# Optimization experiments

Hardware: AMD Instinct MI355X
Metric: run time of the kernel (lower is better)

The kernel has to match this reference:

```python
import jax, jax.numpy as jnp
import numpy as np

NP, NA = 60000, 30000          # paper / author node counts
EC, EW, EB = 300000, 150000, 150000
IN_F, HID, H, D, NCLS = 1024, 512, 4, 128, 153  # HID = H*D


def setup_inputs() -> dict:
    key = jax.random.key(0)
    ks = jax.random.split(key, 24)
    inp = {
        "x_paper": jax.random.normal(ks[0], (NP, IN_F), jnp.float32),
        "x_author": jax.random.normal(ks[1], (NA, IN_F), jnp.float32),
        "cites_src": jax.random.randint(ks[2], (EC,), 0, NP, jnp.int32),
        "cites_dst": jax.random.randint(ks[3], (EC,), 0, NP, jnp.int32),
        "writes_src": jax.random.randint(ks[4], (EW,), 0, NA, jnp.int32),
        "writes_dst": jax.random.randint(ks[5], (EW,), 0, NP, jnp.int32),
        "wb_src": jax.random.randint(ks[6], (EB,), 0, NP, jnp.int32),
        "wb_dst": jax.random.randint(ks[7], (EB,), 0, NA, jnp.int32),
        "W0": jax.random.normal(ks[8], (3, IN_F, HID), jnp.float32) * 0.02,
        "al0": jax.random.normal(ks[9], (3, H, D), jnp.float32) * 0.1,
        "ar0": jax.random.normal(ks[10], (3, H, D), jnp.float32) * 0.1,
        "W1": jax.random.normal(ks[11], (3, HID, HID), jnp.float32) * 0.03,
        "al1": jax.random.normal(ks[12], (3, H, D), jnp.float32) * 0.1,
        "ar1": jax.random.normal(ks[13], (3, H, D), jnp.float32) * 0.1,
        "W2": jax.random.normal(ks[14], (3, HID, HID), jnp.float32) * 0.03,
        "al2": jax.random.normal(ks[15], (3, H, D), jnp.float32) * 0.1,
        "ar2": jax.random.normal(ks[16], (3, H, D), jnp.float32) * 0.1,
        "linW": jax.random.normal(ks[17], (HID, NCLS), jnp.float32) * 0.02,
        "linb": jnp.zeros((NCLS,), jnp.float32),
    }
    return inp


def gat_conv(h_src, h_dst, src, dst, W, al, ar, n_dst):
    """DGL-style GATConv on one edge type (bipartite block, shared fc)."""
    zs = (h_src @ W).reshape(-1, H, D)            # (Ns,H,D)
    zd = (h_dst @ W).reshape(-1, H, D)            # (Nd,H,D)
    el = jnp.sum(zs * al, axis=-1)                # (Ns,H)
    er = jnp.sum(zd * ar, axis=-1)                # (Nd,H)
    e = jax.nn.leaky_relu(el[src] + er[dst], 0.2)  # (E,H)
    # edge softmax over incoming edges per destination node
    m = jax.ops.segment_max(e, dst, num_segments=n_dst)
    m = jnp.where(jnp.isfinite(m), m, 0.0)
    ee = jnp.exp(e - m[dst])
    s = jax.ops.segment_sum(ee, dst, num_segments=n_dst)
    a = ee / (s[dst] + 1e-9)                      # (E,H)
    # weighted message aggregation: (Nd,H,D)
    return jax.ops.segment_sum(a[:, :, None] * zs[src], dst, num_segments=n_dst)


def reference(x_paper, x_author, cites_src, cites_dst, writes_src, writes_dst,
              wb_src, wb_dst, W0, al0, ar0, W1, al1, ar1, W2, al2, ar2,
              linW, linb):
    def hetero_layer(hp, ha, W, al, ar, act):
        # HeteroGraphConv: sum-aggregate per destination node type
        op = (gat_conv(hp, hp, cites_src, cites_dst, W[0], al[0], ar[0], NP)
              + gat_conv(ha, hp, writes_src, writes_dst, W[1], al[1], ar[1], NP))
        oa = gat_conv(hp, ha, wb_src, wb_dst, W[2], al[2], ar[2], NA)
        op = op.reshape(NP, H * D)   # head-flatten as in forward()
        oa = oa.reshape(NA, H * D)
        if act:
            op, oa = jax.nn.relu(op), jax.nn.relu(oa)
        return op, oa

    hp, ha = x_paper, x_author
    hp, ha = hetero_layer(hp, ha, W0, al0, ar0, True)
    hp, ha = hetero_layer(hp, ha, W1, al1, ar1, True)
    hp, ha = hetero_layer(hp, ha, W2, al2, ar2, False)  # last layer: no activation
    return hp @ linW + linb
```

## Files before the change

kernel.cpp:

```cpp
#include <hip/hip_runtime.h>
#include <cstddef>
#include <cstdint>

static constexpr int NP = 60000, NA = 30000;
static constexpr int EC = 300000, EW = 150000, EB = 150000;
static constexpr int IN_F = 1024, HID = 512, H = 4, D = 128, NCLS = 153;
static constexpr int MPAD_P = 60160;
static constexpr int MPAD_A = 30208;

typedef __attribute__((ext_vector_type(8))) short short8;
typedef __attribute__((ext_vector_type(4))) float float4v;

__device__ __forceinline__ unsigned short f2bf(float f) {
    unsigned int u = __float_as_uint(f);
    unsigned int r = u + 0x7FFFu + ((u >> 16) & 1u);
    return (unsigned short)(r >> 16);
}
__device__ __forceinline__ float bf2f(unsigned short h) {
    return __uint_as_float(((unsigned int)h) << 16);
}

__device__ __forceinline__ void gll16(const unsigned short* g, unsigned short* l) {
    __builtin_amdgcn_global_load_lds(
        (const __attribute__((address_space(1))) unsigned int*)g,
        (__attribute__((address_space(3))) unsigned int*)l, 16, 0, 0);
}

__global__ void hist_kernel(const int* __restrict__ dst, int E, int* __restrict__ counts) {
    int e = blockIdx.x * 256 + threadIdx.x;
    if (e < E) atomicAdd(&counts[dst[e]], 1);
}

__global__ void exscan_kernel(const int* __restrict__ in, int* __restrict__ out, int n) {
    __shared__ int wsum[4];
    int t = threadIdx.x;
    int lane = t & 63, w = t >> 6;
    int carry = 0;
    const int CH = 256 * 8;
    for (int base = 0; base < n; base += CH) {
        int v[8], run[8];
        int i0 = base + t * 8;
        int tsum = 0;
#pragma unroll
        for (int j = 0; j < 8; ++j) {
            int i = i0 + j;
            v[j] = (i < n) ? in[i] : 0;
            tsum += v[j];
            run[j] = tsum;
        }
        int x = tsum;
#pragma unroll
        for (int off = 1; off < 64; off <<= 1) {
            int y = __shfl_up(x, off);
            if (lane >= off) x += y;
        }
        if (lane == 63) wsum[w] = x;
        __syncthreads();
        int wpre = 0;
        for (int ww = 0; ww < w; ++ww) wpre += wsum[ww];
        int chunktot = wsum[0] + wsum[1] + wsum[2] + wsum[3];
        int pre = carry + wpre + (x - tsum);
#pragma unroll
        for (int j = 0; j < 8; ++j) {
            int i = i0 + j;
            if (i < n) out[i] = pre + run[j] - v[j];
        }
        carry += chunktot;
        __syncthreads();
    }
    if (t == 0) out[n] = carry;
}

__global__ void fill_kernel(const int* __restrict__ src, const int* __restrict__ dst, int E,
                            int* __restrict__ cursor, int* __restrict__ col) {
    int e = blockIdx.x * 256 + threadIdx.x;
    if (e < E) {
        int pos = atomicAdd(&cursor[dst[e]], 1);
        col[pos] = src[e];
    }
}

__global__ void decomp4_kernel(const float4* __restrict__ x, ushort4* __restrict__ hi,
                               ushort4* __restrict__ lo, int M, int K, int Mpad) {
    size_t i4 = (size_t)blockIdx.x * 256 + threadIdx.x;
    size_t tot = ((size_t)Mpad * K) >> 2;
    if (i4 >= tot) return;
    size_t row = (i4 * 4) / (size_t)K;
    float4 v = make_float4(0.f, 0.f, 0.f, 0.f);
    if (row < (size_t)M) v = x[i4];
    ushort4 h, l;
    h.x = f2bf(v.x); h.y = f2bf(v.y); h.z = f2bf(v.z); h.w = f2bf(v.w);
    l.x = f2bf(v.x - bf2f(h.x)); l.y = f2bf(v.y - bf2f(h.y));
    l.z = f2bf(v.z - bf2f(h.z)); l.w = f2bf(v.w - bf2f(h.w));
    hi[i4] = h; lo[i4] = l;
}

__global__ void btprep_kernel(const float* __restrict__ W, unsigned short* __restrict__ hi,
                              unsigned short* __restrict__ lo, int K, int N, int Npad) {
    int i = blockIdx.x * 256 + threadIdx.x;
    if (i >= Npad * K) return;
    int n = i / K, k = i - n * K;
    float v = (n < N) ? W[(size_t)k * N + n] : 0.f;
    unsigned short h = f2bf(v);
    hi[i] = h;
    lo[i] = f2bf(v - bf2f(h));
}

__global__ __launch_bounds__(512, 2) void gemm_ring(
    const unsigned short* __restrict__ Ahi, const unsigned short* __restrict__ Alo,
    const unsigned short* __restrict__ Bhi, const unsigned short* __restrict__ Blo,
    const float* __restrict__ bias, float* __restrict__ C,
    int M, int K, int Nstore, int ldc) {
    extern __shared__ unsigned short lds[];
    const int tid = threadIdx.x;
    const int lane = tid & 63;
    const int w = tid >> 6;
    const int wr = w >> 2, wc = w & 3;
    const int bm = blockIdx.y * 256, bn = blockIdx.x * 256;

    const int st_row = w * 16 + (lane >> 2);
    const int st_sc = (((lane & 3) ^ ((lane >> 3) & 3)) << 3);
    const size_t aoff0 = (size_t)(bm + st_row) * K + st_sc;
    const size_t aoff1 = aoff0 + (size_t)128 * K;
    const size_t boff0 = (size_t)(bn + st_row) * K + st_sc;
    const size_t boff1 = boff0 + (size_t)128 * K;
    const int ldsA = w * 512;
    const int ldsB = 8192 + w * 512;

    const int arow = wr * 128 + (lane & 15);
    const int brow = wc * 64 + (lane & 15);
    const int rq = ((((lane >> 4) & 3) ^ ((lane >> 1) & 3)) << 3);
    const int aRead = arow * 32 + rq;
    const int bRead = 8192 + brow * 32 + rq;

    float4v acc[8][4];
    float4v zf = {0.f, 0.f, 0.f, 0.f};
#pragma unroll
    for (int i = 0; i < 8; ++i)
#pragma unroll
        for (int j = 0; j < 4; ++j) acc[i][j] = zf;

    auto STAGE = [&](unsigned rr, const unsigned short* As, const unsigned short* Bs, int kc) {
        unsigned short* sb = &lds[rr * 16384u];
        gll16(As + aoff0 + kc, sb + ldsA);
        gll16(As + aoff1 + kc, sb + ldsA + 4096);
        gll16(Bs + boff0 + kc, sb + ldsB);
        gll16(Bs + boff1 + kc, sb + ldsB + 4096);
    };
    auto COMPUTE = [&](unsigned rr) {
        const unsigned short* sb = &lds[rr * 16384u];
        short8 fa[8], fb[4];
#pragma unroll
        for (int i = 0; i < 8; ++i) fa[i] = *(const short8*)&sb[aRead + i * 512];
#pragma unroll
        for (int j = 0; j < 4; ++j) fb[j] = *(const short8*)&sb[bRead + j * 512];
        __builtin_amdgcn_s_setprio(1);
#pragma unroll
        for (int i = 0; i < 8; ++i)
#pragma unroll
            for (int j = 0; j < 4; ++j)
                acc[i][j] = __builtin_amdgcn_mfma_f32_16x16x32_bf16(fa[i], fb[j], acc[i][j], 0, 0, 0);
        __builtin_amdgcn_s_setprio(0);
    };

#define WAITV(n) asm volatile("s_waitcnt vmcnt(" #n ")" ::: "memory")
#define BARF()                                 \
    do {                                       \
        asm volatile("" ::: "memory");         \
        __builtin_amdgcn_s_barrier();          \
        asm volatile("" ::: "memory");         \
    } while (0)

    STAGE(0, Ahi, Bhi, 0);
    STAGE(1, Alo, Bhi, 0);
    STAGE(2, Ahi, Blo, 0);
    unsigned rg = 0;
    const int nK = K >> 5;
#pragma unroll 1
    for (int t3 = 0; t3 < nK - 1; ++t3) {
        const int kn = (t3 + 1) << 5;
        STAGE((rg + 3) & 3, Ahi, Bhi, kn);
        WAITV(12);
        BARF();
        COMPUTE(rg);
        BARF();
        rg = (rg + 1) & 3;
        STAGE((rg + 3) & 3, Alo, Bhi, kn);
        WAITV(12);
        BARF();
        COMPUTE(rg);
        BARF();
        rg = (rg + 1) & 3;
        STAGE((rg + 3) & 3, Ahi, Blo, kn);
        WAITV(12);
        BARF();
        COMPUTE(rg);
        BARF();
        rg = (rg + 1) & 3;
    }
    WAITV(8);
    BARF();
    COMPUTE(rg);
    BARF();
    rg = (rg + 1) & 3;
    WAITV(4);
    BARF();
    COMPUTE(rg);
    BARF();
    rg = (rg + 1) & 3;
    WAITV(0);
    BARF();
    COMPUTE(rg);
#undef WAITV
#undef BARF

    const int col0 = bn + wc * 64 + (lane & 15);
    const int row0 = bm + wr * 128 + ((lane >> 4) << 2);
#pragma unroll
    for (int i = 0; i < 8; ++i) {
#pragma unroll
        for (int j = 0; j < 4; ++j) {
            int col = col0 + j * 16;
            if (col >= Nstore) continue;
            float badd = bias ? bias[col] : 0.f;
            int rowb = row0 + i * 16;
#pragma unroll
            for (int k = 0; k < 4; ++k) {
                int row = rowb + k;
                if (row < M) C[(size_t)row * ldc + col] = acc[i][j][k] + badd;
            }
        }
    }
}

__global__ __launch_bounds__(256) void eler_kernel(
    const float* __restrict__ z, const float* __restrict__ al, const float* __restrict__ ar,
    float* __restrict__ el, float* __restrict__ er, int M) {
    int row = blockIdx.x * 4 + (threadIdx.x >> 6);
    int lane = threadIdx.x & 63;
    if (row >= M) return;
    const float4* zr = (const float4*)(z + (size_t)row * 512 + lane * 8);
    float4 z0 = zr[0], z1 = zr[1];
    const float4* alp = (const float4*)(al + lane * 8);
    float4 a0 = alp[0], a1 = alp[1];
    float s = z0.x * a0.x + z0.y * a0.y + z0.z * a0.z + z0.w * a0.w
            + z1.x * a1.x + z1.y * a1.y + z1.z * a1.z + z1.w * a1.w;
    s += __shfl_xor(s, 8); s += __shfl_xor(s, 4); s += __shfl_xor(s, 2); s += __shfl_xor(s, 1);
    int h = lane >> 4;
    if ((lane & 15) == 0) el[(size_t)row * 4 + h] = s;
    if (er) {
        const float4* arp = (const float4*)(ar + lane * 8);
        float4 b0 = arp[0], b1 = arp[1];
        float t = z0.x * b0.x + z0.y * b0.y + z0.z * b0.z + z0.w * b0.w
                + z1.x * b1.x + z1.y * b1.y + z1.z * b1.z + z1.w * b1.w;
        t += __shfl_xor(t, 8); t += __shfl_xor(t, 4); t += __shfl_xor(t, 2); t += __shfl_xor(t, 1);
        if ((lane & 15) == 0) er[(size_t)row * 4 + h] = t;
    }
}

__global__ void fold_kernel(const float* __restrict__ W, const float* __restrict__ ar,
                            float* __restrict__ v, int K) {
    int i = blockIdx.x * 256 + threadIdx.x;
    if (i >= K * 4) return;
    int k = i >> 2, h = i & 3;
    const float* wr = W + (size_t)k * 512 + h * 128;
    const float* a = ar + h * 128;
    float s = 0.f;
#pragma unroll 4
    for (int d = 0; d < 128; ++d) s += wr[d] * a[d];
    v[i] = s;
}

__global__ __launch_bounds__(256) void skinny_kernel(
    const float* __restrict__ h, const float* __restrict__ v,
    float* __restrict__ er, int M, int K) {
    __shared__ float vs[4096];
    for (int i = threadIdx.x; i < K * 4; i += 256) vs[i] = v[i];
    __syncthreads();
    int row = blockIdx.x * 4 + (threadIdx.x >> 6);
    int lane = threadIdx.x & 63;
    if (row >= M) return;
    const float* hr = h + (size_t)row * K;
    float a0 = 0, a1 = 0, a2 = 0, a3 = 0;
    for (int k = lane; k < K; k += 64) {
        float x = hr[k];
        float4 vv = *(const float4*)&vs[k * 4];
        a0 += x * vv.x; a1 += x * vv.y; a2 += x * vv.z; a3 += x * vv.w;
    }
#pragma unroll
    for (int off = 32; off; off >>= 1) {
        a0 += __shfl_xor(a0, off); a1 += __shfl_xor(a1, off);
        a2 += __shfl_xor(a2, off); a3 += __shfl_xor(a3, off);
    }
    if (lane == 0) *(float4*)&er[(size_t)row * 4] = make_float4(a0, a1, a2, a3);
}

__global__ __launch_bounds__(256) void agg_fused(
    const int* __restrict__ rp1, const int* __restrict__ col1, const float* __restrict__ z1,
    const float* __restrict__ el1, const float* __restrict__ er1,
    const int* __restrict__ rp2, const int* __restrict__ col2, const float* __restrict__ z2,
    const float* __restrict__ el2, const float* __restrict__ er2,
    float* __restrict__ out, unsigned short* __restrict__ hi, unsigned short* __restrict__ lo,
    int N, int do_relu) {
    int j = blockIdx.x * 4 + (threadIdx.x >> 6);
    int lane = threadIdx.x & 63;
    if (j >= N) return;
    int h = lane >> 4;
    float4 acc0 = make_float4(0, 0, 0, 0), acc1 = make_float4(0, 0, 0, 0);

    {
        int e0 = rp1[j], e1 = rp1[j + 1];
        float erh = er1[(size_t)j * 4 + h];
        float m = -INFINITY, s = 0.f;
        for (int e = e0; e < e1; ++e) {
            float x = el1[(size_t)col1[e] * 4 + h] + erh;
            x = (x >= 0.f) ? x : 0.2f * x;
            float mn = fmaxf(m, x);
            s = s * expf(m - mn) + expf(x - mn);
            m = mn;
        }
        float inv = 1.0f / (s + 1e-9f);
        for (int e = e0; e < e1; ++e) {
            int src = col1[e];
            float x = el1[(size_t)src * 4 + h] + erh;
            x = (x >= 0.f) ? x : 0.2f * x;
            float wgt = expf(x - m) * inv;
            const float4* zr = (const float4*)(z1 + (size_t)src * 512 + lane * 8);
            float4 za = zr[0], zb = zr[1];
            acc0.x += wgt * za.x; acc0.y += wgt * za.y; acc0.z += wgt * za.z; acc0.w += wgt * za.w;
            acc1.x += wgt * zb.x; acc1.y += wgt * zb.y; acc1.z += wgt * zb.z; acc1.w += wgt * zb.w;
        }
    }
    if (rp2) {
        int e0 = rp2[j], e1 = rp2[j + 1];
        float erh = er2[(size_t)j * 4 + h];
        float m = -INFINITY, s = 0.f;
        for (int e = e0; e < e1; ++e) {
            float x = el2[(size_t)col2[e] * 4 + h] + erh;
            x = (x >= 0.f) ? x : 0.2f * x;
            float mn = fmaxf(m, x);
            s = s * expf(m - mn) + expf(x - mn);
            m = mn;
        }
        float inv = 1.0f / (s + 1e-9f);
        for (int e = e0; e < e1; ++e) {
            int src = col2[e];
            float x = el2[(size_t)src * 4 + h] + erh;
            x = (x >= 0.f) ? x : 0.2f * x;
            float wgt = expf(x - m) * inv;
            const float4* zr = (const float4*)(z2 + (size_t)src * 512 + lane * 8);
            float4 za = zr[0], zb = zr[1];
            acc0.x += wgt * za.x; acc0.y += wgt * za.y; acc0.z += wgt * za.z; acc0.w += wgt * za.w;
            acc1.x += wgt * zb.x; acc1.y += wgt * zb.y; acc1.z += wgt * zb.z; acc1.w += wgt * zb.w;
        }
    }
    if (do_relu) {
        acc0.x = fmaxf(acc0.x, 0.f); acc0.y = fmaxf(acc0.y, 0.f);
        acc0.z = fmaxf(acc0.z, 0.f); acc0.w = fmaxf(acc0.w, 0.f);
        acc1.x = fmaxf(acc1.x, 0.f); acc1.y = fmaxf(acc1.y, 0.f);
        acc1.z = fmaxf(acc1.z, 0.f); acc1.w = fmaxf(acc1.w, 0.f);
    }
    float* op = out + (size_t)j * 512 + lane * 8;
    *(float4*)op = acc0;
    *(float4*)(op + 4) = acc1;
    if (hi) {
        size_t base = (size_t)j * 512 + lane * 8;
        ushort4 h0, h1, l0, l1;
        h0.x = f2bf(acc0.x); h0.y = f2bf(acc0.y); h0.z = f2bf(acc0.z); h0.w = f2bf(acc0.w);
        h1.x = f2bf(acc1.x); h1.y = f2bf(acc1.y); h1.z = f2bf(acc1.z); h1.w = f2bf(acc1.w);
        l0.x = f2bf(acc0.x - bf2f(h0.x)); l0.y = f2bf(acc0.y - bf2f(h0.y));
        l0.z = f2bf(acc0.z - bf2f(h0.z)); l0.w = f2bf(acc0.w - bf2f(h0.w));
        l1.x = f2bf(acc1.x - bf2f(h1.x)); l1.y = f2bf(acc1.y - bf2f(h1.y));
        l1.z = f2bf(acc1.z - bf2f(h1.z)); l1.w = f2bf(acc1.w - bf2f(h1.w));
        *(ushort4*)(hi + base) = h0;
        *(ushort4*)(hi + base + 4) = h1;
        *(ushort4*)(lo + base) = l0;
        *(ushort4*)(lo + base + 4) = l1;
    }
}

extern "C" void kernel_launch(void* const* d_in, const int* in_sizes, int n_in,
                              void* d_out, int out_size, void* d_ws, size_t ws_size,
                              hipStream_t stream) {
    const float* x_paper = (const float*)d_in[0];
    const float* x_author = (const float*)d_in[1];
    const int* cites_src = (const int*)d_in[2];
    const int* cites_dst = (const int*)d_in[3];
    const int* writes_src = (const int*)d_in[4];
    const int* writes_dst = (const int*)d_in[5];
    const int* wb_src = (const int*)d_in[6];
    const int* wb_dst = (const int*)d_in[7];
    const float* W0 = (const float*)d_in[8];
    const float* al0 = (const float*)d_in[9];
    const float* ar0 = (const float*)d_in[10];
    const float* W1 = (const float*)d_in[11];
    const float* al1 = (const float*)d_in[12];
    const float* ar1 = (const float*)d_in[13];
    const float* W2 = (const float*)d_in[14];
    const float* al2 = (const float*)d_in[15];
    const float* ar2 = (const float*)d_in[16];
    const float* linW = (const float*)d_in[17];
    const float* linb = (const float*)d_in[18];
    float* out = (float*)d_out;

    (void)hipFuncSetAttribute((const void*)gemm_ring,
                              hipFuncAttributeMaxDynamicSharedMemorySize, 131072);

    char* p = (char*)d_ws;
    auto alloc = [&](size_t n) { char* r = p; p += (n + 255) & ~(size_t)255; return r; };

    float* hpA = (float*)alloc((size_t)NP * 512 * 4);
    float* hpB = (float*)alloc((size_t)NP * 512 * 4);
    float* haA = (float*)alloc((size_t)NA * 512 * 4);
    float* haB = (float*)alloc((size_t)NA * 512 * 4);
    float* zbuf = (float*)alloc((size_t)NP * 512 * 4);
    float* elA = (float*)alloc((size_t)NP * 16);
    float* erA = (float*)alloc((size_t)NP * 16);
    float* elB = (float*)alloc((size_t)NP * 16);
    float* erB = (float*)alloc((size_t)NP * 16);
    float* vfold = (float*)alloc(4096 * 4);
    int* rp_c = (int*)alloc((NP + 1) * 4);
    int* col_c = (int*)alloc((size_t)EC * 4);
    int* rp_w = (int*)alloc((NP + 1) * 4);
    int* col_w = (int*)alloc((size_t)EW * 4);
    int* rp_b = (int*)alloc((NA + 1) * 4);
    int* col_b = (int*)alloc((size_t)EB * 4);
    int* cursor = (int*)alloc((NP + 1) * 4);
    int* counts = (int*)alloc((size_t)NP * 4);

    unsigned short* AhiP = (unsigned short*)alloc((size_t)MPAD_P * 1024 * 2);
    unsigned short* AloP = (unsigned short*)alloc((size_t)MPAD_P * 1024 * 2);
    unsigned short* AhiA = (unsigned short*)alloc((size_t)MPAD_A * 1024 * 2);
    unsigned short* AloA = (unsigned short*)alloc((size_t)MPAD_A * 1024 * 2);
    const int Ks[3] = {IN_F, HID, HID};
    unsigned short *bthi[3][3], *btlo[3][3];
    for (int l = 0; l < 3; ++l)
        for (int t = 0; t < 3; ++t) {
            bthi[l][t] = (unsigned short*)alloc((size_t)512 * Ks[l] * 2);
            btlo[l][t] = (unsigned short*)alloc((size_t)512 * Ks[l] * 2);
        }
    unsigned short* btLhi = (unsigned short*)alloc((size_t)256 * 512 * 2);
    unsigned short* btLlo = (unsigned short*)alloc((size_t)256 * 512 * 2);
    (void)ws_size;

    struct EdgeT { const int* src; const int* dst; int E; int n; int* rp; int* col; };
    EdgeT ets[3] = {
        {cites_src, cites_dst, EC, NP, rp_c, col_c},
        {writes_src, writes_dst, EW, NP, rp_w, col_w},
        {wb_src, wb_dst, EB, NA, rp_b, col_b},
    };
    for (int t = 0; t < 3; ++t) {
        hipMemsetAsync(counts, 0, (size_t)ets[t].n * 4, stream);
        hist_kernel<<<(ets[t].E + 255) / 256, 256, 0, stream>>>(ets[t].dst, ets[t].E, counts);
        exscan_kernel<<<1, 256, 0, stream>>>(counts, ets[t].rp, ets[t].n);
        hipMemcpyAsync(cursor, ets[t].rp, (size_t)ets[t].n * 4, hipMemcpyDeviceToDevice, stream);
        fill_kernel<<<(ets[t].E + 255) / 256, 256, 0, stream>>>(ets[t].src, ets[t].dst, ets[t].E, cursor, ets[t].col);
    }

    const float* Wl[3] = {W0, W1, W2};
    const float* alL[3] = {al0, al1, al2};
    const float* arL[3] = {ar0, ar1, ar2};

    for (int l = 0; l < 3; ++l) {
        int K = Ks[l];
        for (int t = 0; t < 3; ++t)
            btprep_kernel<<<(512 * K + 255) / 256, 256, 0, stream>>>(
                Wl[l] + (size_t)t * K * 512, bthi[l][t], btlo[l][t], K, 512, 512);
    }
    btprep_kernel<<<(256 * 512 + 255) / 256, 256, 0, stream>>>(linW, btLhi, btLlo, 512, NCLS, 256);

    decomp4_kernel<<<((size_t)MPAD_P * 1024 / 4 + 255) / 256, 256, 0, stream>>>(
        (const float4*)x_paper, (ushort4*)AhiP, (ushort4*)AloP, NP, 1024, MPAD_P);
    decomp4_kernel<<<((size_t)MPAD_A * 1024 / 4 + 255) / 256, 256, 0, stream>>>(
        (const float4*)x_author, (ushort4*)AhiA, (ushort4*)AloA, NA, 1024, MPAD_A);

    auto gemm = [&](const unsigned short* Ah, const unsigned short* Al,
                    const unsigned short* Bh, const unsigned short* Bl,
                    const float* bias, float* C, int M, int Mpad, int K, int gx,
                    int Nstore, int ldc) {
        dim3 g(gx, Mpad / 256);
        gemm_ring<<<g, 512, 131072, stream>>>(Ah, Al, Bh, Bl, bias, C, M, K, Nstore, ldc);
    };

    const float* hp = x_paper;
    const float* ha = x_author;
    for (int l = 0; l < 3; ++l) {
        int K = Ks[l];
        float* hp_n = (l & 1) ? hpB : hpA;
        float* ha_n = (l & 1) ? haB : haA;
        float* zbuf_w = ha_n;
        const float* W = Wl[l];
        const float* al = alL[l];
        const float* ar = arL[l];
        size_t wstride = (size_t)K * 512;
        int relu = (l < 2) ? 1 : 0;

        gemm(AhiP, AloP, bthi[l][0], btlo[l][0], nullptr, zbuf, NP, MPAD_P, K, 2, 512, 512);
        gemm(AhiA, AloA, bthi[l][1], btlo[l][1], nullptr, zbuf_w, NA, MPAD_A, K, 2, 512, 512);
        eler_kernel<<<(NP + 3) / 4, 256, 0, stream>>>(zbuf, al, ar, elA, erA, NP);
        eler_kernel<<<(NA + 3) / 4, 256, 0, stream>>>(zbuf_w, al + 512, nullptr, elB, nullptr, NA);
        fold_kernel<<<(K * 4 + 255) / 256, 256, 0, stream>>>(W + wstride, ar + 512, vfold, K);
        skinny_kernel<<<(NP + 3) / 4, 256, 0, stream>>>(hp, vfold, erB, NP, K);
        agg_fused<<<(NP + 3) / 4, 256, 0, stream>>>(
            rp_c, col_c, zbuf, elA, erA,
            rp_w, col_w, zbuf_w, elB, erB,
            hp_n, nullptr, nullptr, NP, relu);
        gemm(AhiP, AloP, bthi[l][2], btlo[l][2], nullptr, zbuf, NP, MPAD_P, K, 2, 512, 512);
        decomp4_kernel<<<((size_t)MPAD_P * 512 / 4 + 255) / 256, 256, 0, stream>>>(
            (const float4*)hp_n, (ushort4*)AhiP, (ushort4*)AloP, NP, 512, MPAD_P);
        eler_kernel<<<(NP + 3) / 4, 256, 0, stream>>>(zbuf, al + 1024, nullptr, elA, nullptr, NP);
        fold_kernel<<<(K * 4 + 255) / 256, 256, 0, stream>>>(W + 2 * wstride, ar + 1024, vfold, K);
        skinny_kernel<<<(NA + 3) / 4, 256, 0, stream>>>(ha, vfold, erA, NA, K);
        agg_fused<<<(NA + 3) / 4, 256, 0, stream>>>(
            rp_b, col_b, zbuf, elA, erA,
            nullptr, nullptr, nullptr, nullptr, nullptr,
            ha_n, (l < 2) ? AhiA : nullptr, (l < 2) ? AloA : nullptr, NA, relu);
        hp = hp_n;
        ha = ha_n;
    }
    gemm(AhiP, AloP, btLhi, btLlo, linb, out, NP, MPAD_P, 512, 1, NCLS, NCLS);
}
```

Baseline: 3.377 ms.

## Split GEMM tile into two phases interleaving LDS reads, global stages and MFMAs

```diff
diff --git a/kernel.cpp b/kernel.cpp
--- a/kernel.cpp
+++ b/kernel.cpp
@@ -106,7 +106,7 @@
     lo[i] = f2bf(v - bf2f(h));
 }
 
-__global__ __launch_bounds__(512, 2) void gemm_ring(
+__global__ __launch_bounds__(512, 2) void gemm_8ph(
     const unsigned short* __restrict__ Ahi, const unsigned short* __restrict__ Alo,
     const unsigned short* __restrict__ Bhi, const unsigned short* __restrict__ Blo,
     const float* __restrict__ bias, float* __restrict__ C,
@@ -140,27 +140,12 @@
 #pragma unroll
         for (int j = 0; j < 4; ++j) acc[i][j] = zf;
 
-    auto STAGE = [&](unsigned rr, const unsigned short* As, const unsigned short* Bs, int kc) {
+    auto STAGE_ALL = [&](unsigned rr, const unsigned short* As, const unsigned short* Bs, int kc) {
         unsigned short* sb = &lds[rr * 16384u];
         gll16(As + aoff0 + kc, sb + ldsA);
         gll16(As + aoff1 + kc, sb + ldsA + 4096);
         gll16(Bs + boff0 + kc, sb + ldsB);
         gll16(Bs + boff1 + kc, sb + ldsB + 4096);
-    };
-    auto COMPUTE = [&](unsigned rr) {
-        const unsigned short* sb = &lds[rr * 16384u];
-        short8 fa[8], fb[4];
-#pragma unroll
-        for (int i = 0; i < 8; ++i) fa[i] = *(const short8*)&sb[aRead + i * 512];
-#pragma unroll
-        for (int j = 0; j < 4; ++j) fb[j] = *(const short8*)&sb[bRead + j * 512];
-        __builtin_amdgcn_s_setprio(1);
-#pragma unroll
-        for (int i = 0; i < 8; ++i)
-#pragma unroll
-            for (int j = 0; j < 4; ++j)
-                acc[i][j] = __builtin_amdgcn_mfma_f32_16x16x32_bf16(fa[i], fb[j], acc[i][j], 0, 0, 0);
-        __builtin_amdgcn_s_setprio(0);
     };
 
 #define WAITV(n) asm volatile("s_waitcnt vmcnt(" #n ")" ::: "memory")
@@ -171,46 +156,67 @@
         asm volatile("" ::: "memory");         \
     } while (0)
 
-    STAGE(0, Ahi, Bhi, 0);
-    STAGE(1, Alo, Bhi, 0);
-    STAGE(2, Ahi, Blo, 0);
+#define TILE(RR, ASRC, BSRC, KN, DOSTAGE, WAITSTMT)                                   \
+    do {                                                                              \
+        const unsigned short* sb = &lds[(RR) * 16384u];                               \
+        unsigned short* db = &lds[(((RR) + 3u) & 3u) * 16384u];                       \
+        short8 fa[4], fb[4];                                                          \
+        _Pragma("unroll") for (int i = 0; i < 4; ++i)                                 \
+            fa[i] = *(const short8*)&sb[aRead + i * 512];                             \
+        _Pragma("unroll") for (int j = 0; j < 4; ++j)                                 \
+            fb[j] = *(const short8*)&sb[bRead + j * 512];                             \
+        if (DOSTAGE) {                                                                \
+            gll16(ASRC + aoff0 + (KN), db + ldsA);                                    \
+            gll16(ASRC + aoff1 + (KN), db + ldsA + 4096);                             \
+        }                                                                             \
+        BARF();                                                                       \
+        __builtin_amdgcn_s_setprio(1);                                                \
+        _Pragma("unroll") for (int i = 0; i < 4; ++i)                                 \
+            _Pragma("unroll") for (int j = 0; j < 4; ++j)                             \
+                acc[i][j] = __builtin_amdgcn_mfma_f32_16x16x32_bf16(fa[i], fb[j], acc[i][j], 0, 0, 0); \
+        __builtin_amdgcn_s_setprio(0);                                                \
+        BARF();                                                                       \
+        short8 fa2[4];                                                                \
+        _Pragma("unroll") for (int i = 0; i < 4; ++i)                                 \
+            fa2[i] = *(const short8*)&sb[aRead + (i + 4) * 512];                      \
+        if (DOSTAGE) {                                                                \
+            gll16(BSRC + boff0 + (KN), db + ldsB);                                    \
+            gll16(BSRC + boff1 + (KN), db + ldsB + 4096);                             \
+        }                                                                             \
+        BARF();                                                                       \
+        __builtin_amdgcn_s_setprio(1);                                                \
+        _Pragma("unroll") for (int i = 0; i < 4; ++i)                                 \
+            _Pragma("unroll") for (int j = 0; j < 4; ++j)                             \
+                acc[i + 4][j] = __builtin_amdgcn_mfma_f32_16x16x32_bf16(fa2[i], fb[j], acc[i + 4][j], 0, 0, 0); \
+        __builtin_amdgcn_s_setprio(0);                                                \
+        WAITSTMT;                                                                     \
+        BARF();                                                                       \
+    } while (0)
+
+    STAGE_ALL(0, Ahi, Bhi, 0);
+    STAGE_ALL(1, Alo, Bhi, 0);
+    STAGE_ALL(2, Ahi, Blo, 0);
+    WAITV(8);
+    BARF();
+
     unsigned rg = 0;
     const int nK = K >> 5;
 #pragma unroll 1
-    for (int t3 = 0; t3 < nK - 1; ++t3) {
-        const int kn = (t3 + 1) << 5;
-        STAGE((rg + 3) & 3, Ahi, Bhi, kn);
-        WAITV(12);
-        BARF();
-        COMPUTE(rg);
-        BARF();
+    for (int c = 0; c < nK - 1; ++c) {
+        const int kn = (c + 1) << 5;
+        TILE(rg, Ahi, Bhi, kn, 1, WAITV(8));
         rg = (rg + 1) & 3;
-        STAGE((rg + 3) & 3, Alo, Bhi, kn);
-        WAITV(12);
-        BARF();
-        COMPUTE(rg);
-        BARF();
+        TILE(rg, Alo, Bhi, kn, 1, WAITV(8));
         rg = (rg + 1) & 3;
-        STAGE((rg + 3) & 3, Ahi, Blo, kn);
-        WAITV(12);
-        BARF();
-        COMPUTE(rg);
-        BARF();
+        TILE(rg, Ahi, Blo, kn, 1, WAITV(8));
         rg = (rg + 1) & 3;
     }
-    WAITV(8);
-    BARF();
-    COMPUTE(rg);
-    BARF();
+    TILE(rg, Ahi, Bhi, 0, 0, WAITV(4));
     rg = (rg + 1) & 3;
-    WAITV(4);
-    BARF();
-    COMPUTE(rg);
-    BARF();
+    TILE(rg, Alo, Bhi, 0, 0, WAITV(0));
     rg = (rg + 1) & 3;
-    WAITV(0);
-    BARF();
-    COMPUTE(rg);
+    TILE(rg, Ahi, Blo, 0, 0, (void)0);
+#undef TILE
 #undef WAITV
 #undef BARF
 
@@ -358,7 +364,7 @@
         acc0.x = fmaxf(acc0.x, 0.f); acc0.y = fmaxf(acc0.y, 0.f);
         acc0.z = fmaxf(acc0.z, 0.f); acc0.w = fmaxf(acc0.w, 0.f);
         acc1.x = fmaxf(acc1.x, 0.f); acc1.y = fmaxf(acc1.y, 0.f);
-        acc1.z = fmaxf(acc1.z, 0.f); acc1.w = fmaxf(acc1.w, 0.f);
+        acc1.w = fmaxf(acc1.w, 0.f); acc1.z = fmaxf(acc1.z, 0.f);
     }
     float* op = out + (size_t)j * 512 + lane * 8;
     *(float4*)op = acc0;
@@ -403,7 +409,7 @@
     const float* linb = (const float*)d_in[18];
     float* out = (float*)d_out;
 
-    (void)hipFuncSetAttribute((const void*)gemm_ring,
+    (void)hipFuncSetAttribute((const void*)gemm_8ph,
                               hipFuncAttributeMaxDynamicSharedMemorySize, 131072);
 
     char* p = (char*)d_ws;
@@ -479,7 +485,7 @@
                     const float* bias, float* C, int M, int Mpad, int K, int gx,
                     int Nstore, int ldc) {
         dim3 g(gx, Mpad / 256);
-        gemm_ring<<<g, 512, 131072, stream>>>(Ah, Al, Bh, Bl, bias, C, M, K, Nstore, ldc);
+        gemm_8ph<<<g, 512, 131072, stream>>>(Ah, Al, Bh, Bl, bias, C, M, K, Nstore, ldc);
     };
 
     const float* hp = x_paper;
```

New measurement: 3.318 ms. Within noise of the previous version (-1.8%).
